# Optimization experiments

Measured on AMD Instinct MI355X. Metric: run time of the kernel, lower is better.

Reference implementation:

```python
import jax, jax.numpy as jnp
import numpy as np

N, FIN, H, M = 20000, 64, 128, 16
EIA, EIR, EIT = 256000, 256000, 100000
EIN = 2 * H + 1          # EGNN edge-mlp input: feats_i | feats_j | rel_dist
EHID = 2 * EIN
NIN = H + M
NHID = 2 * H


def _gat(x_src, x_dst, ei, w_src, w_dst, a_s, a_d, b):
    # PyG GATConv, heads=1: alpha_ij = softmax_i(leaky_relu(a_s.Wx_j + a_d.Wx_i))
    n_dst = x_dst.shape[0]
    h_s = x_src @ w_src                      # [Ns, H]
    h_d = x_dst @ w_dst                      # [Nd, H]
    es = h_s @ a_s                           # [Ns]
    ed = h_d @ a_d                           # [Nd]
    j, i = ei[0], ei[1]                      # src, dst
    e = jax.nn.leaky_relu(es[j] + ed[i], 0.2)
    mx = jax.ops.segment_max(e, i, num_segments=n_dst)
    mx = jnp.where(jnp.isfinite(mx), mx, 0.0)  # guard empty segments
    ex = jnp.exp(e - mx[i])
    den = jax.ops.segment_sum(ex, i, num_segments=n_dst)
    alpha = ex / (den[i] + 1e-16)
    return jax.ops.segment_sum(alpha[:, None] * h_s[j], i, num_segments=n_dst) + b


def _egnn(x, ei, p):
    # EGNN_Sparse: x = [coors(3) | feats], 'add' aggregation, residual feat update
    ew1, eb1, ew2, eb2, cw1, cb1, cw2, cb2, nw1, nb1, nw2, nb2 = p
    coors, feats = x[:, :3], x[:, 3:]
    n = x.shape[0]
    j, i = ei[0], ei[1]
    rel = coors[j] - coors[i]                          # [E, 3] (src - dst)
    rd = jnp.sum(rel * rel, axis=-1, keepdims=True)    # [E, 1]
    m_in = jnp.concatenate([feats[i], feats[j], rd], axis=-1)
    m = jax.nn.silu(jax.nn.silu(m_in @ ew1 + eb1) @ ew2 + eb2)   # [E, M]
    cw = jax.nn.silu(m @ cw1 + cb1) @ cw2 + cb2                  # [E, 1]
    coors_out = coors + jax.ops.segment_sum(cw * rel, i, num_segments=n)
    m_i = jax.ops.segment_sum(m, i, num_segments=n)
    feats_out = feats + jax.nn.silu(jnp.concatenate([feats, m_i], axis=-1) @ nw1 + nb1) @ nw2 + nb2
    return jnp.concatenate([coors_out, feats_out], axis=-1)


def setup_inputs():
    ks = iter(jax.random.split(jax.random.key(0), 48))

    def nrm(shape, s=0.1):
        return jax.random.normal(next(ks), shape, dtype=jnp.float32) * s

    def ridx(shape):
        return jax.random.randint(next(ks), shape, 0, N, dtype=jnp.int32)

    return {
        "x1": nrm((N, FIN), 1.0), "x2": nrm((N, FIN), 1.0),
        "pos1": nrm((N, 3), 1.0), "pos2": nrm((N, 3), 1.0),
        "ei_intra1": ridx((2, EIA)), "ei_intra2": ridx((2, EIA)),
        "ei_12": ridx((2, EIR)), "ei_21": ridx((2, EIR)),
        "ei_int": ridx((2, EIT)),
        "g0_w": nrm((2, FIN, H)), "g0_as": nrm((2, H)), "g0_ad": nrm((2, H)), "g0_b": nrm((2, H)),
        "g1_w": nrm((2, H, H)), "g1_as": nrm((2, H)), "g1_ad": nrm((2, H)), "g1_b": nrm((2, H)),
        "it_ws": nrm((2, 2, H, H)), "it_wd": nrm((2, 2, H, H)),
        "it_as": nrm((2, 2, H)), "it_ad": nrm((2, 2, H)), "it_b": nrm((2, 2, H)),
        "eg_e_w1": nrm((2, 2, EIN, EHID)), "eg_e_b1": nrm((2, 2, EHID)),
        "eg_e_w2": nrm((2, 2, EHID, M)), "eg_e_b2": nrm((2, 2, M)),
        "eg_c_w1": nrm((2, 2, M, 4 * M)), "eg_c_b1": nrm((2, 2, 4 * M)),
        "eg_c_w2": nrm((2, 2, 4 * M, 1)), "eg_c_b2": nrm((2, 2, 1)),
        "eg_n_w1": nrm((2, 2, NIN, NHID)), "eg_n_b1": nrm((2, 2, NHID)),
        "eg_n_w2": nrm((2, 2, NHID, H)), "eg_n_b2": nrm((2, 2, H)),
        "lin_w": nrm((H, 1)), "lin_b": nrm((1,)),
        "aux_w1": nrm((2 * H, H)), "aux_b1": nrm((H,)),
        "aux_w2": nrm((H, 1)), "aux_b2": nrm((1,)),
    }


def reference(x1, x2, pos1, pos2,
              g0_w, g0_as, g0_ad, g0_b, g1_w, g1_as, g1_ad, g1_b,
              it_ws, it_wd, it_as, it_ad, it_b,
              eg_e_w1, eg_e_b1, eg_e_w2, eg_e_b2, eg_c_w1, eg_c_b1, eg_c_w2, eg_c_b2,
              eg_n_w1, eg_n_b1, eg_n_w2, eg_n_b2,
              lin_w, lin_b, aux_w1, aux_b1, aux_w2, aux_b2,
              ei_intra1, ei_intra2, ei_12, ei_21, ei_int):
    n1, n2 = x1.shape[0], x2.shape[0]
    sl1 = jnp.tile(jnp.arange(n1, dtype=ei_intra1.dtype)[None, :], (2, 1))
    sl2 = jnp.tile(jnp.arange(n2, dtype=ei_intra2.dtype)[None, :], (2, 1))
    ei1 = jnp.concatenate([ei_intra1, sl1], axis=1)  # GATConv add_self_loops=True
    ei2 = jnp.concatenate([ei_intra2, sl2], axis=1)
    # intra GAT layers (shared lin for src/dst)
    x1 = jax.nn.relu(_gat(x1, x1, ei1, g0_w[0], g0_w[0], g0_as[0], g0_ad[0], g0_b[0]))
    x2 = jax.nn.relu(_gat(x2, x2, ei2, g0_w[1], g0_w[1], g0_as[1], g0_ad[1], g0_b[1]))
    x1 = jax.nn.relu(_gat(x1, x1, ei1, g1_w[0], g1_w[0], g1_as[0], g1_ad[0], g1_b[0]))
    x2 = jax.nn.relu(_gat(x2, x2, ei2, g1_w[1], g1_w[1], g1_as[1], g1_ad[1], g1_b[1]))
    # inter GAT layers (bipartite, add_self_loops=False)
    for l in range(2):
        nx2 = jax.nn.relu(_gat(x1, x2, ei_12, it_ws[l, 0], it_wd[l, 0], it_as[l, 0], it_ad[l, 0], it_b[l, 0]))
        nx1 = jax.nn.relu(_gat(x2, x1, ei_21, it_ws[l, 1], it_wd[l, 1], it_as[l, 1], it_ad[l, 1], it_b[l, 1]))
        x1, x2 = nx1, nx2
    # EGNN layers (HeteroEGNN hstacks pos only when feat dim == node_dim, i.e. layer 0)
    egp = (eg_e_w1, eg_e_b1, eg_e_w2, eg_e_b2, eg_c_w1, eg_c_b1, eg_c_w2, eg_c_b2,
           eg_n_w1, eg_n_b1, eg_n_w2, eg_n_b2)
    h1 = jnp.concatenate([pos1, x1], axis=-1)
    h2 = jnp.concatenate([pos2, x2], axis=-1)
    for l in range(2):
        h1 = _egnn(h1, ei_intra1, tuple(p[l, 0] for p in egp))
        h2 = _egnn(h2, ei_intra2, tuple(p[l, 1] for p in egp))
    x1, x2 = h1[:, 3:], h2[:, 3:]
    # auxiliary distance head on interacting pairs
    xi = jnp.concatenate([x1[ei_int[0]], x2[ei_int[1]]], axis=-1)
    dist = jax.nn.relu(jax.nn.relu(xi @ aux_w1 + aux_b1) @ aux_w2 + aux_b2)
    return (x1 @ lin_w + lin_b, x2 @ lin_w + lin_b, dist)
```

## Files before the change

### kernel.cpp

```cpp
#include <hip/hip_runtime.h>
#include <hip/hip_bf16.h>
#include <cstdint>
#include <cstddef>

#define NN     20000
#define FIN_D  64
#define H_D    128
#define M_D    16
#define EIA_D  256000
#define EIR_D  256000
#define EIT_D  100000
#define EIN_D  257
#define EHID_D 514
#define NIN_D  144
#define NHID_D 256
#define APAD   544
#define BUPAD  272

typedef short bfrag __attribute__((ext_vector_type(8)));
typedef float ffrag __attribute__((ext_vector_type(4)));

__device__ __forceinline__ float siluf(float x) {
    return x * __builtin_amdgcn_rcpf(1.f + __expf(-x));
}
__device__ __forceinline__ float reluf(float x) { return x > 0.f ? x : 0.f; }
__device__ __forceinline__ unsigned short f2bf(float f) {
    unsigned u = __float_as_uint(f);
    return (unsigned short)((u + 0x7FFFu + ((u >> 16) & 1u)) >> 16);
}
__device__ __forceinline__ float bf2f(unsigned short h) { return __uint_as_float(((unsigned)h) << 16); }
__device__ __forceinline__ float bf_lo(unsigned u) { return __uint_as_float(u << 16); }
__device__ __forceinline__ float bf_hi(unsigned u) { return __uint_as_float(u & 0xFFFF0000u); }
__device__ __forceinline__ unsigned pkbf(float f0, float f1) {
    __hip_bfloat162 h = __float22bfloat162_rn(make_float2(f0, f1));
    return *(unsigned*)&h;
}

__global__ void k_filli(int* p, int v, int n) {
    int i = blockIdx.x * 256 + threadIdx.x; if (i < n) p[i] = v;
}
__global__ void k_iota(int* p, int n) {
    int i = blockIdx.x * 256 + threadIdx.x; if (i < n) p[i] = i;
}
__global__ void k_hist(const int* __restrict__ si, int nE, int* __restrict__ cnt) {
    int e = blockIdx.x * 256 + threadIdx.x; if (e < nE) atomicAdd(&cnt[si[e]], 1);
}
__global__ void k_scan4(const int* __restrict__ cnt4, int n, int* __restrict__ rp4) {
    const int* cnt = cnt4 + (size_t)blockIdx.x * n;
    int* rp = rp4 + (size_t)blockIdx.x * (n + 1);
    __shared__ int tmp[256];
    __shared__ int carry;
    if (threadIdx.x == 0) { carry = 0; rp[0] = 0; }
    __syncthreads();
    for (int base = 0; base < n; base += 256) {
        int i = base + threadIdx.x;
        int v = (i < n) ? cnt[i] : 0;
        tmp[threadIdx.x] = v;
        __syncthreads();
        for (int off = 1; off < 256; off <<= 1) {
            int t = (threadIdx.x >= off) ? tmp[threadIdx.x - off] : 0;
            __syncthreads();
            tmp[threadIdx.x] += t;
            __syncthreads();
        }
        if (i < n) rp[i + 1] = carry + tmp[threadIdx.x];
        __syncthreads();
        if (threadIdx.x == 0) carry += tmp[255];
        __syncthreads();
    }
}
__global__ void k_scatter(const int* __restrict__ sj, const int* __restrict__ si, int nE,
                          const int* __restrict__ rp, int* __restrict__ cursor,
                          int* __restrict__ colj, int* __restrict__ dsti) {
    int e = blockIdx.x * 256 + threadIdx.x;
    if (e >= nE) return;
    int i = si[e];
    int p = rp[i] + atomicAdd(&cursor[i], 1);
    colj[p] = sj[e];
    if (dsti) dsti[p] = i;
}

struct PrepDesc { const float* src; unsigned dstOff; int K, N, Kpad, Npad; };
struct PrepArgs { PrepDesc d[29]; };
__global__ void k_prep(PrepArgs pa, unsigned short* __restrict__ Wt) {
    PrepDesc de = pa.d[blockIdx.x];
    int tot = de.Npad * de.Kpad;
    unsigned short* hi = Wt + de.dstOff;
    unsigned short* lo = hi + tot;
    for (int i = blockIdx.y * 256 + threadIdx.x; i < tot; i += gridDim.y * 256) {
        int n = i / de.Kpad, k = i - n * de.Kpad;
        float v = (n < de.N && k < de.K) ? de.src[(size_t)k * de.N + n] : 0.f;
        unsigned short h = f2bf(v);
        hi[i] = h;
        lo[i] = f2bf(v - bf2f(h));
    }
}

__global__ void k_prep_ew2(const float* __restrict__ eg_e_w2, const float* __restrict__ eg_c_w1,
                           unsigned short* __restrict__ Wf) {
    int pidx = blockIdx.x;
    const float* src = eg_e_w2 + (size_t)pidx * EHID_D * M_D;
    unsigned short* hi = Wf + (size_t)pidx * 8704;
    unsigned short* lo = Wf + 4 * 8704 + (size_t)pidx * 8704;
    for (int idx = threadIdx.x; idx < 8704; idx += 256) {
        int t = idx >> 9, rem = idx & 511;
        int lane = rem >> 3, j2 = rem & 7;
        int k = t * 32 + ((lane >> 4) << 3) + j2;
        int n = lane & 15;
        float v = (k < EHID_D) ? src[(size_t)k * 16 + n] : 0.f;
        unsigned short h = f2bf(v);
        hi[idx] = h;
        lo[idx] = f2bf(v - bf2f(h));
    }
    const float* cw1 = eg_c_w1 + (size_t)pidx * 16 * 64;
    unsigned short* ghi = Wf + 69632 + (size_t)pidx * 4096;
    unsigned short* glo = ghi + 2048;
    for (int idx = threadIdx.x; idx < 2048; idx += 256) {
        int nt = idx >> 9, rem = idx & 511;
        int lane = rem >> 3, j = rem & 7;
        int q = lane >> 4, mm = lane & 15;
        int k = q * 8 + j;
        float v = (k < 16) ? cw1[(size_t)k * 64 + nt * 16 + mm] : 0.f;
        unsigned short h = f2bf(v);
        ghi[idx] = h;
        glo[idx] = f2bf(v - bf2f(h));
    }
}

struct MMJob {
    const float* A; const float* A2;
    const int* gi0; const int* gi1;
    const unsigned short* Wh; const unsigned short* Wl;
    const float* bias; const float* res;
    float* C; unsigned short* C2;
    const float* da; const float* db;
    float* dota; float* dotb;
};
struct MMJobs { MMJob j[4]; };

template<int ACT, bool OBF, int DOT, bool NOC, int KT>
__global__ __launch_bounds__(256) void k_mmf(MMJobs js, int M, int Nc, int ldc, int nbn) {
    constexpr int K = KT * 32;
    __shared__ __align__(16) unsigned short sAh[128 * K];
    const MMJob jb = js.j[blockIdx.z];
    const int tid = threadIdx.x;
    const int bm = blockIdx.x * 128;
    const int wv = tid >> 6, lane = tid & 63;
    const int q = lane >> 4, mm = lane & 15;
    const int sr = tid >> 1;
    const int sks = (tid & 1) * 16;
    const int gm_s = bm + sr;
    const int sgmt = sr >> 4, smm = sr & 15, qb = (tid & 1) * 2;
#pragma unroll
    for (int t = 0; t < KT; ++t) {
        float v[16];
        if (gm_s < M) {
            const float* src = jb.A + (size_t)gm_s * K + t * 32 + sks;
#pragma unroll
            for (int i = 0; i < 4; ++i) {
                float4 t4 = ((const float4*)src)[i];
                v[4 * i] = t4.x; v[4 * i + 1] = t4.y; v[4 * i + 2] = t4.z; v[4 * i + 3] = t4.w;
            }
        } else {
#pragma unroll
            for (int i = 0; i < 16; ++i) v[i] = 0.f;
        }
#pragma unroll
        for (int o = 0; o < 2; ++o) {
            unsigned hw[4];
#pragma unroll
            for (int p = 0; p < 4; ++p)
                hw[p] = pkbf(v[o * 8 + 2 * p], v[o * 8 + 2 * p + 1]);
            int off16 = ((sgmt * KT + t) * 4 + qb + o) * 16 + smm;
            ((uint4*)sAh)[off16] = make_uint4(hw[0], hw[1], hw[2], hw[3]);
        }
    }
    __syncthreads();
    float dra[2][4] = {}, drb[2][4] = {};
    for (int b = 0; b < nbn; ++b) {
        const int bn = b * 64;
        ffrag acc[2][4];
#pragma unroll
        for (int mt = 0; mt < 2; ++mt)
#pragma unroll
            for (int nt = 0; nt < 4; ++nt)
#pragma unroll
                for (int r = 0; r < 4; ++r) acc[mt][nt][r] = 0.f;
#pragma unroll
        for (int t = 0; t < KT; ++t) {
            bfrag bh[4], bl[4];
#pragma unroll
            for (int nt = 0; nt < 4; ++nt) {
                size_t woff = (size_t)(bn + nt * 16 + mm) * K + t * 32 + q * 8;
                bh[nt] = *(const bfrag*)(jb.Wh + woff);
                bl[nt] = *(const bfrag*)(jb.Wl + woff);
            }
#pragma unroll
            for (int mt = 0; mt < 2; ++mt) {
                int off16 = (((wv * 2 + mt) * KT + t) * 4 + q) * 16 + mm;
                bfrag ah = ((const bfrag*)sAh)[off16];
#pragma unroll
                for (int nt = 0; nt < 4; ++nt) {
                    acc[mt][nt] = __builtin_amdgcn_mfma_f32_16x16x32_bf16(ah, bh[nt], acc[mt][nt], 0, 0, 0);
                    acc[mt][nt] = __builtin_amdgcn_mfma_f32_16x16x32_bf16(ah, bl[nt], acc[mt][nt], 0, 0, 0);
                }
            }
        }
        if (DOT >= 1) {
            float dav[4], dbv[4];
#pragma unroll
            for (int nt = 0; nt < 4; ++nt) {
                int gn = bn + nt * 16 + mm;
                dav[nt] = (gn < Nc) ? jb.da[gn] : 0.f;
                if (DOT == 2) dbv[nt] = (gn < Nc) ? jb.db[gn] : 0.f;
            }
#pragma unroll
            for (int mt = 0; mt < 2; ++mt)
#pragma unroll
                for (int r = 0; r < 4; ++r)
#pragma unroll
                    for (int nt = 0; nt < 4; ++nt) {
                        dra[mt][r] += acc[mt][nt][r] * dav[nt];
                        if (DOT == 2) drb[mt][r] += acc[mt][nt][r] * dbv[nt];
                    }
        }
        const bool doC2 = jb.C2 != nullptr;
        if (!NOC || doC2) {
#pragma unroll
            for (int mt = 0; mt < 2; ++mt) {
#pragma unroll
                for (int nt = 0; nt < 4; ++nt) {
                    int gn = bn + nt * 16 + mm;
                    bool inb = gn < Nc;
                    bool padz = OBF && !NOC && !inb && gn < ldc;
                    if (!inb && !padz) continue;
#pragma unroll
                    for (int r = 0; r < 4; ++r) {
                        int gm = bm + wv * 32 + mt * 16 + q * 4 + r;
                        if (gm >= M) continue;
                        if (padz) {
                            ((unsigned short*)jb.C)[(size_t)gm * ldc + gn] = 0;
                            continue;
                        }
                        float vv = acc[mt][nt][r];
                        if (jb.bias) vv += jb.bias[gn];
                        if (ACT == 1) vv = reluf(vv);
                        if (ACT == 2) vv = siluf(vv);
                        if (!NOC) {
                            if (OBF) ((unsigned short*)jb.C)[(size_t)gm * ldc + gn] = f2bf(vv);
                            else jb.C[(size_t)gm * ldc + gn] = vv;
                        }
                        if (doC2) jb.C2[(size_t)gm * ldc + gn] = f2bf(vv);
                    }
                }
            }
        }
    }
    if (DOT >= 1) {
#pragma unroll
        for (int mt = 0; mt < 2; ++mt)
#pragma unroll
            for (int r = 0; r < 4; ++r) {
                float sa = dra[mt][r];
                sa += __shfl_xor(sa, 1); sa += __shfl_xor(sa, 2);
                sa += __shfl_xor(sa, 4); sa += __shfl_xor(sa, 8);
                float sb = 0.f;
                if (DOT == 2) {
                    sb = drb[mt][r];
                    sb += __shfl_xor(sb, 1); sb += __shfl_xor(sb, 2);
                    sb += __shfl_xor(sb, 4); sb += __shfl_xor(sb, 8);
                }
                int gm = bm + wv * 32 + mt * 16 + q * 4 + r;
                if (mm == 0 && gm < M) {
                    jb.dota[gm] = sa;
                    if (DOT == 2) jb.dotb[gm] = sb;
                }
            }
    }
}

template<int ACT, bool RES, bool GATHER>
__global__ __launch_bounds__(256) void k_mm(MMJobs js, int M, int Nc, int K, int Kpad, int ldc, int s2) {
    __shared__ __align__(16) unsigned short sAh[128 * 32];
    __shared__ __align__(16) unsigned short sAl[128 * 32];
    const MMJob jb = js.j[blockIdx.z];
    const int tid = threadIdx.x;
    const int bm = blockIdx.x * 128, bn = blockIdx.y * 64;
    const int wv = tid >> 6, lane = tid & 63;
    ffrag acc[2][4];
#pragma unroll
    for (int mt = 0; mt < 2; ++mt)
#pragma unroll
        for (int nt = 0; nt < 4; ++nt)
#pragma unroll
            for (int r = 0; r < 4; ++r) acc[mt][nt][r] = 0.f;
    const int sr = tid >> 1;
    const int sks = (tid & 1) * 16;
    const int gm_s = bm + sr;
    const int sgmt = sr >> 4, smm = sr & 15, qb = (tid & 1) * 2;
    int gidx0 = 0, gidx1 = 0;
    if (GATHER && gm_s < M) { gidx0 = jb.gi0[gm_s]; gidx1 = jb.gi1[gm_s]; }
    const int q = lane >> 4, mm = lane & 15;

    for (int k0 = 0; k0 < Kpad; k0 += 32) {
        float v[16];
        bool valid = (gm_s < M) && (k0 + sks < K);
        if (valid) {
            const float* src;
            int kk = k0 + sks;
            if (GATHER) src = (kk < 128) ? (jb.A + (size_t)gidx0 * 128 + kk)
                                         : (jb.A2 + (size_t)gidx1 * s2 + (kk - 128));
            else src = jb.A + (size_t)gm_s * K + kk;
#pragma unroll
            for (int i = 0; i < 4; ++i) {
                float4 t4 = ((const float4*)src)[i];
                v[4 * i] = t4.x; v[4 * i + 1] = t4.y; v[4 * i + 2] = t4.z; v[4 * i + 3] = t4.w;
            }
        } else {
#pragma unroll
            for (int i = 0; i < 16; ++i) v[i] = 0.f;
        }
#pragma unroll
        for (int o = 0; o < 2; ++o) {
            unsigned hw[4], lw[4];
#pragma unroll
            for (int p = 0; p < 4; ++p) {
                float f0 = v[o * 8 + 2 * p], f1 = v[o * 8 + 2 * p + 1];
                unsigned short h0 = f2bf(f0), h1 = f2bf(f1);
                unsigned short l0 = f2bf(f0 - bf2f(h0)), l1 = f2bf(f1 - bf2f(h1));
                hw[p] = (unsigned)h0 | ((unsigned)h1 << 16);
                lw[p] = (unsigned)l0 | ((unsigned)l1 << 16);
            }
            int off16 = (sgmt * 4 + qb + o) * 16 + smm;
            ((uint4*)sAh)[off16] = make_uint4(hw[0], hw[1], hw[2], hw[3]);
            ((uint4*)sAl)[off16] = make_uint4(lw[0], lw[1], lw[2], lw[3]);
        }
        __syncthreads();
        bfrag bh[4], bl[4];
#pragma unroll
        for (int nt = 0; nt < 4; ++nt) {
            size_t woff = (size_t)(bn + nt * 16 + mm) * Kpad + k0 + q * 8;
            bh[nt] = *(const bfrag*)(jb.Wh + woff);
            bl[nt] = *(const bfrag*)(jb.Wl + woff);
        }
#pragma unroll
        for (int mt = 0; mt < 2; ++mt) {
            int off16 = ((wv * 2 + mt) * 4 + q) * 16 + mm;
            bfrag ah = ((const bfrag*)sAh)[off16];
            bfrag al = ((const bfrag*)sAl)[off16];
#pragma unroll
            for (int nt = 0; nt < 4; ++nt) {
                acc[mt][nt] = __builtin_amdgcn_mfma_f32_16x16x32_bf16(ah, bh[nt], acc[mt][nt], 0, 0, 0);
                acc[mt][nt] = __builtin_amdgcn_mfma_f32_16x16x32_bf16(ah, bl[nt], acc[mt][nt], 0, 0, 0);
                acc[mt][nt] = __builtin_amdgcn_mfma_f32_16x16x32_bf16(al, bh[nt], acc[mt][nt], 0, 0, 0);
            }
        }
        __syncthreads();
    }
#pragma unroll
    for (int mt = 0; mt < 2; ++mt) {
#pragma unroll
        for (int nt = 0; nt < 4; ++nt) {
            int gn = bn + nt * 16 + mm;
            if (gn >= Nc) continue;
#pragma unroll
            for (int r = 0; r < 4; ++r) {
                int gm = bm + wv * 32 + mt * 16 + q * 4 + r;
                if (gm >= M) continue;
                float vv = acc[mt][nt][r];
                if (jb.bias) vv += jb.bias[gn];
                if (ACT == 1) vv = reluf(vv);
                if (ACT == 2) vv = siluf(vv);
                if (RES) vv += jb.res[(size_t)gm * Nc + gn];
                jb.C[(size_t)gm * ldc + gn] = vv;
            }
        }
    }
}

__global__ void k_nodescore(const float* __restrict__ x, const float* __restrict__ wv,
                            const float* __restrict__ b, float* __restrict__ o, int n) {
    int w = blockIdx.x * 4 + (threadIdx.x >> 6);
    int lane = threadIdx.x & 63;
    if (w >= n) return;
    const float* r = x + (size_t)w * H_D;
    float s = r[lane] * wv[lane] + r[lane + 64] * wv[lane + 64];
#pragma unroll
    for (int off = 32; off; off >>= 1) s += __shfl_xor(s, off);
    if (lane == 0) o[w] = s + b[0];
}

struct GatJob {
    const int* rp; const int* cj; int hasSelf;
    const float* es; const float* ed;
    const unsigned* h16; const float* bias; float* out;
};
__global__ __launch_bounds__(256) void k_gat2(GatJob j0, GatJob j1, int N) {
    const GatJob jb = blockIdx.y ? j1 : j0;
    int node = blockIdx.x * 4 + (threadIdx.x >> 6);
    int lane = threadIdx.x & 63;
    if (node >= N) return;
    int start = jb.rp[node], end = jb.rp[node + 1];
    float edi = jb.ed[node];
    float den = 0.f, a0 = 0.f, a1 = 0.f;
    int p = start;
    for (; p + 4 <= end; p += 4) {
        int j[4]; float e[4]; unsigned u[4];
#pragma unroll
        for (int x = 0; x < 4; ++x) j[x] = jb.cj[p + x];
#pragma unroll
        for (int x = 0; x < 4; ++x) { e[x] = jb.es[j[x]]; u[x] = jb.h16[(size_t)j[x] * 64 + lane]; }
#pragma unroll
        for (int x = 0; x < 4; ++x) {
            float v = e[x] + edi;
            v = v < 0.f ? 0.2f * v : v;
            float ex = __expf(v);
            den += ex;
            a0 += ex * bf_lo(u[x]);
            a1 += ex * bf_hi(u[x]);
        }
    }
    for (; p < end; ++p) {
        int j = jb.cj[p];
        float v = jb.es[j] + edi;
        v = v < 0.f ? 0.2f * v : v;
        float ex = __expf(v);
        den += ex;
        unsigned u = jb.h16[(size_t)j * 64 + lane];
        a0 += ex * bf_lo(u);
        a1 += ex * bf_hi(u);
    }
    if (jb.hasSelf) {
        float v = jb.es[node] + edi;
        v = v < 0.f ? 0.2f * v : v;
        float ex = __expf(v);
        den += ex;
        unsigned u = jb.h16[(size_t)node * 64 + lane];
        a0 += ex * bf_lo(u);
        a1 += ex * bf_hi(u);
    }
    float inv = 1.f / (den + 1e-16f);
    float2 o;
    o.x = reluf(a0 * inv + jb.bias[2 * lane]);
    o.y = reluf(a1 * inv + jb.bias[2 * lane + 1]);
    ((float2*)(jb.out + (size_t)node * H_D))[lane] = o;
}

struct EJob {
    const int* dsti; const int* cj;
    const unsigned* A16; const unsigned* Bp; const float* coors;
    const float* w_rd;
    const unsigned short* Wfh; const unsigned short* Wfl;
    const unsigned short* Wgh; const unsigned short* Wgl;
    const float* eb2; const float* cb1;
    const float* cw2; const float* cb2;
    unsigned short* me16; float* cvec;
};
__global__ __launch_bounds__(256) void k_edge2(EJob e0, EJob e1, int nE) {
    const EJob jb = blockIdx.y ? e1 : e0;
    __shared__ __align__(16) float s_w[APAD];
    __shared__ float s_cb1[64], s_cw2[64], s_eb2[16];
    __shared__ __align__(16) float sM[4][16][20];
    for (int i = threadIdx.x; i < APAD; i += 256)
        s_w[i] = (i < EHID_D) ? jb.w_rd[i] : 0.f;
    if (threadIdx.x < 64) { s_cb1[threadIdx.x] = jb.cb1[threadIdx.x]; s_cw2[threadIdx.x] = jb.cw2[threadIdx.x]; }
    if (threadIdx.x < 16) s_eb2[threadIdx.x] = jb.eb2[threadIdx.x];
    __syncthreads();
    const float cb2v = jb.cb2[0];
    const int wv = threadIdx.x >> 6, lane = threadIdx.x & 63;
    const int q = lane >> 4, mm = lane & 15;
    const int ebase = blockIdx.x * 64 + wv * 16;
    const int e = ebase + mm;
    const bool ev = e < nE;
    int ii = ev ? jb.dsti[e] : 0;
    int jj = ev ? jb.cj[e] : 0;
    float dx = jb.coors[(size_t)jj * 3]     - jb.coors[(size_t)ii * 3];
    float dy = jb.coors[(size_t)jj * 3 + 1] - jb.coors[(size_t)ii * 3 + 1];
    float dz = jb.coors[(size_t)jj * 3 + 2] - jb.coors[(size_t)ii * 3 + 2];
    float rd = dx * dx + dy * dy + dz * dz;
    const unsigned* Ar = jb.A16 + (size_t)ii * BUPAD;
    const unsigned* Br = jb.Bp + (size_t)jj * BUPAD;
    ffrag acc = {0.f, 0.f, 0.f, 0.f};
#pragma unroll 4
    for (int t = 0; t < 17; ++t) {
        int ks = t * 32 + q * 8;
        int ku = ks >> 1;
        uint4 au = *(const uint4*)(Ar + ku);
        uint4 bu = *(const uint4*)(Br + ku);
        float4 w0 = *(const float4*)(s_w + ks);
        float4 w1 = *(const float4*)(s_w + ks + 4);
        float g[8];
        g[0] = siluf(bf_lo(au.x) + bf_lo(bu.x) + rd * w0.x);
        g[1] = siluf(bf_hi(au.x) + bf_hi(bu.x) + rd * w0.y);
        g[2] = siluf(bf_lo(au.y) + bf_lo(bu.y) + rd * w0.z);
        g[3] = siluf(bf_hi(au.y) + bf_hi(bu.y) + rd * w0.w);
        g[4] = siluf(bf_lo(au.z) + bf_lo(bu.z) + rd * w1.x);
        g[5] = siluf(bf_hi(au.z) + bf_hi(bu.z) + rd * w1.y);
        g[6] = siluf(bf_lo(au.w) + bf_lo(bu.w) + rd * w1.z);
        g[7] = siluf(bf_hi(au.w) + bf_hi(bu.w) + rd * w1.w);
        bfrag ah;
        unsigned* ahp = (unsigned*)&ah;
        ahp[0] = pkbf(g[0], g[1]);
        ahp[1] = pkbf(g[2], g[3]);
        ahp[2] = pkbf(g[4], g[5]);
        ahp[3] = pkbf(g[6], g[7]);
        bfrag bh = *(const bfrag*)(jb.Wfh + (size_t)(t * 64 + lane) * 8);
        bfrag bl = *(const bfrag*)(jb.Wfl + (size_t)(t * 64 + lane) * 8);
        acc = __builtin_amdgcn_mfma_f32_16x16x32_bf16(ah, bh, acc, 0, 0, 0);
        acc = __builtin_amdgcn_mfma_f32_16x16x32_bf16(ah, bl, acc, 0, 0, 0);
    }
#pragma unroll
    for (int r = 0; r < 4; ++r) {
        int erow = q * 4 + r;
        float me = siluf(acc[r] + s_eb2[mm]);
        sM[wv][erow][mm] = me;
        int e2 = ebase + erow;
        if (e2 < nE) jb.me16[(size_t)e2 * 16 + mm] = f2bf(me);
    }
    bfrag ag;
    unsigned* agp = (unsigned*)&ag;
    if (q < 2) {
        float4 m0 = *(const float4*)&sM[wv][mm][q * 8];
        float4 m1 = *(const float4*)&sM[wv][mm][q * 8 + 4];
        agp[0] = pkbf(m0.x, m0.y);
        agp[1] = pkbf(m0.z, m0.w);
        agp[2] = pkbf(m1.x, m1.y);
        agp[3] = pkbf(m1.z, m1.w);
    } else {
        agp[0] = agp[1] = agp[2] = agp[3] = 0u;
    }
    float part[4] = {0.f, 0.f, 0.f, 0.f};
#pragma unroll
    for (int nt = 0; nt < 4; ++nt) {
        bfrag gh = *(const bfrag*)(jb.Wgh + (size_t)(nt * 64 + lane) * 8);
        bfrag gl = *(const bfrag*)(jb.Wgl + (size_t)(nt * 64 + lane) * 8);
        ffrag a2 = {0.f, 0.f, 0.f, 0.f};
        a2 = __builtin_amdgcn_mfma_f32_16x16x32_bf16(ag, gh, a2, 0, 0, 0);
        a2 = __builtin_amdgcn_mfma_f32_16x16x32_bf16(ag, gl, a2, 0, 0, 0);
        int n = nt * 16 + mm;
        float c1 = s_cb1[n], c2 = s_cw2[n];
#pragma unroll
        for (int r = 0; r < 4; ++r) part[r] += siluf(a2[r] + c1) * c2;
    }
#pragma unroll
    for (int r = 0; r < 4; ++r) {
        part[r] += __shfl_xor(part[r], 1);
        part[r] += __shfl_xor(part[r], 2);
        part[r] += __shfl_xor(part[r], 4);
        part[r] += __shfl_xor(part[r], 8);
    }
    int srcl = (lane >> 2) << 4;
    float cand0 = __shfl(part[0], srcl);
    float cand1 = __shfl(part[1], srcl);
    float cand2 = __shfl(part[2], srcl);
    float cand3 = __shfl(part[3], srcl);
    if (lane < 16) {
        int rr = lane & 3;
        float cwv = (rr == 0 ? cand0 : rr == 1 ? cand1 : rr == 2 ? cand2 : cand3) + cb2v;
        int e3 = ebase + lane;
        if (e3 < nE) {
            jb.cvec[(size_t)e3 * 3]     = cwv * dx;
            jb.cvec[(size_t)e3 * 3 + 1] = cwv * dy;
            jb.cvec[(size_t)e3 * 3 + 2] = cwv * dz;
        }
    }
}

struct SJob {
    const int* rp; const unsigned short* me16; const float* cvec;
    const float* coors; float* coorsOut; float* macc;
};
__global__ __launch_bounds__(256) void k_seg2(SJob s0, SJob s1, int N) {
    const SJob jb = blockIdx.y ? s1 : s0;
    int node = blockIdx.x * 4 + (threadIdx.x >> 6);
    int lane = threadIdx.x & 63;
    if (node >= N) return;
    int s = jb.rp[node], en = jb.rp[node + 1];
    int x = lane >> 4, c = lane & 15;
    float msum = 0.f, csum = 0.f;
    for (int p = s + x; p < en; p += 4) {
        msum += bf2f(jb.me16[(size_t)p * 16 + c]);
        if (c < 3) csum += jb.cvec[(size_t)p * 3 + c];
    }
    msum += __shfl_xor(msum, 16); msum += __shfl_xor(msum, 32);
    csum += __shfl_xor(csum, 16); csum += __shfl_xor(csum, 32);
    if (lane < 16) jb.macc[(size_t)node * M_D + lane] = msum;
    if (lane < 3) jb.coorsOut[(size_t)node * 3 + lane] = jb.coors[(size_t)node * 3 + lane] + csum;
}

__global__ void k_dist(const float* __restrict__ Hb, const float* __restrict__ w2,
                       const float* __restrict__ b2, float* __restrict__ dist, int nE) {
    int e = blockIdx.x * 4 + (threadIdx.x >> 6);
    int lane = threadIdx.x & 63;
    if (e >= nE) return;
    const float* r = Hb + (size_t)e * H_D;
    float s = r[lane] * w2[lane] + r[lane + 64] * w2[lane + 64];
#pragma unroll
    for (int off = 32; off; off >>= 1) s += __shfl_xor(s, off);
    if (lane == 0) dist[e] = reluf(s + b2[0]);
}

extern "C" void kernel_launch(void* const* d_in, const int* in_sizes, int n_in,
                              void* d_out, int out_size, void* d_ws, size_t ws_size,
                              hipStream_t stream) {
    const float* x1_in = (const float*)d_in[0];
    const float* x2_in = (const float*)d_in[1];
    const float* pos1  = (const float*)d_in[2];
    const float* pos2  = (const float*)d_in[3];
    const int* ei_intra1 = (const int*)d_in[4];
    const int* ei_intra2 = (const int*)d_in[5];
    const int* ei_12 = (const int*)d_in[6];
    const int* ei_21 = (const int*)d_in[7];
    const int* ei_int = (const int*)d_in[8];
    const float* g0_w  = (const float*)d_in[9];
    const float* g0_as = (const float*)d_in[10];
    const float* g0_ad = (const float*)d_in[11];
    const float* g0_b  = (const float*)d_in[12];
    const float* g1_w  = (const float*)d_in[13];
    const float* g1_as = (const float*)d_in[14];
    const float* g1_ad = (const float*)d_in[15];
    const float* g1_b  = (const float*)d_in[16];
    const float* it_ws = (const float*)d_in[17];
    const float* it_wd = (const float*)d_in[18];
    const float* it_as = (const float*)d_in[19];
    const float* it_ad = (const float*)d_in[20];
    const float* it_b  = (const float*)d_in[21];
    const float* eg_e_w1 = (const float*)d_in[22];
    const float* eg_e_b1 = (const float*)d_in[23];
    const float* eg_e_w2 = (const float*)d_in[24];
    const float* eg_e_b2 = (const float*)d_in[25];
    const float* eg_c_w1 = (const float*)d_in[26];
    const float* eg_c_b1 = (const float*)d_in[27];
    const float* eg_c_w2 = (const float*)d_in[28];
    const float* eg_c_b2 = (const float*)d_in[29];
    const float* eg_n_w1 = (const float*)d_in[30];
    const float* eg_n_b1 = (const float*)d_in[31];
    const float* eg_n_w2 = (const float*)d_in[32];
    const float* eg_n_b2 = (const float*)d_in[33];
    const float* lin_w = (const float*)d_in[34];
    const float* lin_b = (const float*)d_in[35];
    const float* aux_w1 = (const float*)d_in[36];
    const float* aux_b1 = (const float*)d_in[37];
    const float* aux_w2 = (const float*)d_in[38];
    const float* aux_b2 = (const float*)d_in[39];
    float* dout = (float*)d_out;

    float* wsf = (float*)d_ws;
    size_t off = 0;
    auto alloc = [&](size_t nfl) { float* p = wsf + off; off += (nfl + 255) & ~(size_t)255; return p; };
    float* x1a = alloc((size_t)NN * H_D);
    float* x2a = alloc((size_t)NN * H_D);
    float* x1b = alloc((size_t)NN * H_D);
    float* x2b = alloc((size_t)NN * H_D);
    float* esed = alloc(4 * NN);
    float* es1 = esed, *es2 = esed + NN, *ed1 = esed + 2 * NN, *ed2 = esed + 3 * NN;
    float* co1a = alloc(NN * 3);
    float* co1b = alloc(NN * 3);
    float* co2a = alloc(NN * 3);
    float* co2b = alloc(NN * 3);
    float* macc1 = alloc((size_t)NN * M_D);
    float* macc2 = alloc((size_t)NN * M_D);
    unsigned* A16a = (unsigned*)alloc((size_t)NN * BUPAD);
    unsigned* B16a = (unsigned*)alloc((size_t)NN * BUPAD);
    unsigned* A16b = (unsigned*)alloc((size_t)NN * BUPAD);
    unsigned* B16b = (unsigned*)alloc((size_t)NN * BUPAD);
    unsigned* h16a = (unsigned*)alloc((size_t)NN * 64);
    unsigned* h16b = (unsigned*)alloc((size_t)NN * 64);
    int* cnt4 = (int*)alloc(4 * NN);
    int* rp4 = (int*)alloc(4 * (NN + 1));
    int* cjI1 = (int*)alloc(EIA_D);
    int* cjI2 = (int*)alloc(EIA_D);
    int* cj12 = (int*)alloc(EIR_D);
    int* cj21 = (int*)alloc(EIR_D);
    int* dstI1 = (int*)alloc(EIA_D);
    int* dstI2 = (int*)alloc(EIA_D);
    int* iota = (int*)alloc(NN);
    unsigned short* Wt = (unsigned short*)alloc(1100000);
    unsigned short* Wf = (unsigned short*)alloc(45000);
    unsigned short* me16a = (unsigned short*)alloc((size_t)EIA_D * 8);
    unsigned short* me16b = (unsigned short*)alloc((size_t)EIA_D * 8);
    float* cveca = alloc((size_t)EIA_D * 3);
    float* cvecb = alloc((size_t)EIA_D * 3);
    float* nh1 = (float*)B16a;
    float* nh2 = (float*)B16b;
    float* Hb  = (float*)A16a;

    const int N = NN, H = H_D;
    int gNW = (N + 3) / 4;
    int gEA = (EIA_D + 255) / 256;

    PrepArgs pa;
    unsigned woffs[29], wsz[29];
    unsigned wo = 0;
    int wi = 0;
    auto addw = [&](const float* src, int K, int Ncols) {
        int Kpad = (K + 31) & ~31;
        int Npad = (Ncols + 63) & ~63;
        pa.d[wi] = {src, wo, K, Ncols, Kpad, Npad};
        woffs[wi] = wo; wsz[wi] = (unsigned)(Npad * Kpad);
        wo += 2u * Npad * Kpad;
        ++wi;
    };
    addw(g0_w, FIN_D, H);
    addw(g0_w + FIN_D * H, FIN_D, H);
    addw(g1_w, H, H);
    addw(g1_w + H * H, H, H);
    for (int p = 0; p < 4; ++p) addw(it_ws + (size_t)p * H * H, H, H);
    for (int p = 0; p < 4; ++p) addw(it_wd + (size_t)p * H * H, H, H);
    for (int p = 0; p < 4; ++p) {
        const float* ew1 = eg_e_w1 + (size_t)p * EIN_D * EHID_D;
        addw(ew1, H, EHID_D);
        addw(ew1 + (size_t)H * EHID_D, H, EHID_D);
    }
    for (int p = 0; p < 4; ++p) addw(eg_n_w1 + (size_t)p * NIN_D * NHID_D, NIN_D, NHID_D);
    for (int p = 0; p < 4; ++p) addw(eg_n_w2 + (size_t)p * NHID_D * H, NHID_D, H);
    addw(aux_w1, 2 * H, H);
    k_prep<<<dim3(29, 16), 256, 0, stream>>>(pa, Wt);
    k_prep_ew2<<<4, 256, 0, stream>>>(eg_e_w2, eg_c_w1, Wf);
    auto WH = [&](int i) { return (const unsigned short*)(Wt + woffs[i]); };
    auto WL = [&](int i) { return (const unsigned short*)(Wt + woffs[i] + wsz[i]); };

    k_filli<<<(4 * N + 255) / 256, 256, 0, stream>>>(cnt4, 0, 4 * N);
    k_iota<<<(N + 255) / 256, 256, 0, stream>>>(iota, N);
    k_hist<<<gEA, 256, 0, stream>>>(ei_intra1 + EIA_D, EIA_D, cnt4);
    k_hist<<<gEA, 256, 0, stream>>>(ei_intra2 + EIA_D, EIA_D, cnt4 + N);
    k_hist<<<gEA, 256, 0, stream>>>(ei_12 + EIR_D, EIR_D, cnt4 + 2 * N);
    k_hist<<<gEA, 256, 0, stream>>>(ei_21 + EIR_D, EIR_D, cnt4 + 3 * N);
    k_scan4<<<4, 256, 0, stream>>>(cnt4, N, rp4);
    k_filli<<<(4 * N + 255) / 256, 256, 0, stream>>>(cnt4, 0, 4 * N);
    const int* rpI1 = rp4;
    const int* rpI2 = rp4 + (N + 1);
    const int* rp12 = rp4 + 2 * (N + 1);
    const int* rp21 = rp4 + 3 * (N + 1);
    k_scatter<<<gEA, 256, 0, stream>>>(ei_intra1, ei_intra1 + EIA_D, EIA_D, rpI1, cnt4, cjI1, dstI1);
    k_scatter<<<gEA, 256, 0, stream>>>(ei_intra2, ei_intra2 + EIA_D, EIA_D, rpI2, cnt4 + N, cjI2, dstI2);
    k_scatter<<<gEA, 256, 0, stream>>>(ei_12, ei_12 + EIR_D, EIR_D, rp12, cnt4 + 2 * N, cj12, nullptr);
    k_scatter<<<gEA, 256, 0, stream>>>(ei_21, ei_21 + EIR_D, EIR_D, rp21, cnt4 + 3 * N, cj21, nullptr);

    const int MB = (N + 127) / 128;
    MMJobs js{};

    auto intraL = [&](auto kt_tag, const float* xa, const float* xb, int wa, int wb,
                      const float* as_a, const float* ad_a, const float* as_b, const float* ad_b,
                      const float* b_a, const float* b_b, float* oa, float* ob) {
        constexpr int KT = decltype(kt_tag)::value;
        js.j[0] = {xa, nullptr, nullptr, nullptr, WH(wa), WL(wa), nullptr, nullptr,
                   nullptr, (unsigned short*)h16a, as_a, ad_a, es1, ed1};
        js.j[1] = {xb, nullptr, nullptr, nullptr, WH(wb), WL(wb), nullptr, nullptr,
                   nullptr, (unsigned short*)h16b, as_b, ad_b, es2, ed2};
        k_mmf<0, false, 2, true, KT><<<dim3(MB, 1, 2), 256, 0, stream>>>(js, N, H, H, 2);
        GatJob g0{rpI1, cjI1, 1, es1, ed1, h16a, b_a, oa};
        GatJob g1{rpI2, cjI2, 1, es2, ed2, h16b, b_b, ob};
        k_gat2<<<dim3(gNW, 2), 256, 0, stream>>>(g0, g1, N);
    };

    intraL(std::integral_constant<int, 2>{}, x1_in, x2_in, 0, 1,
           g0_as, g0_ad, g0_as + H, g0_ad + H, g0_b, g0_b + H, x1a, x2a);
    const float* cx1 = x1a;
    const float* cx2 = x2a;
    intraL(std::integral_constant<int, 4>{}, cx1, cx2, 2, 3,
           g1_as, g1_ad, g1_as + H, g1_ad + H, g1_b, g1_b + H, x1b, x2b);
    cx1 = x1b; cx2 = x2b;

    {
        float* outs1[2] = {x1a, x1b};
        float* outs2[2] = {x2a, x2b};
        for (int l = 0; l < 2; ++l) {
            int p0 = l * 2 + 0, p1 = l * 2 + 1;
            float* o2 = outs2[l];
            float* o1 = outs1[l];
            js.j[0] = {cx1, nullptr, nullptr, nullptr, WH(4 + p0), WL(4 + p0), nullptr, nullptr,
                       nullptr, (unsigned short*)h16a, it_as + p0 * H, nullptr, es1, nullptr};
            js.j[1] = {cx2, nullptr, nullptr, nullptr, WH(4 + p1), WL(4 + p1), nullptr, nullptr,
                       nullptr, (unsigned short*)h16b, it_as + p1 * H, nullptr, es2, nullptr};
            js.j[2] = {cx2, nullptr, nullptr, nullptr, WH(8 + p0), WL(8 + p0), nullptr, nullptr,
                       nullptr, nullptr, it_ad + p0 * H, nullptr, ed1, nullptr};
            js.j[3] = {cx1, nullptr, nullptr, nullptr, WH(8 + p1), WL(8 + p1), nullptr, nullptr,
                       nullptr, nullptr, it_ad + p1 * H, nullptr, ed2, nullptr};
            k_mmf<0, false, 1, true, 4><<<dim3(MB, 1, 4), 256, 0, stream>>>(js, N, H, H, 2);
            GatJob g0{rp12, cj12, 0, es1, ed1, h16a, it_b + p0 * H, o2};
            GatJob g1{rp21, cj21, 0, es2, ed2, h16b, it_b + p1 * H, o1};
            k_gat2<<<dim3(gNW, 2), 256, 0, stream>>>(g0, g1, N);
            cx1 = o1; cx2 = o2;
        }
    }

    auto egnn_pair = [&](const float* f1, const float* f2, const float* c1, const float* c2,
                         int l, float* fo1, float* fo2, float* co1, float* co2) {
        int p0 = 2 * l, p1 = 2 * l + 1;
        js.j[0] = {f1, nullptr, nullptr, nullptr, WH(12 + 2 * p0), WL(12 + 2 * p0),
                   eg_e_b1 + p0 * EHID_D, nullptr, (float*)A16a, nullptr, nullptr, nullptr, nullptr, nullptr};
        js.j[1] = {f1, nullptr, nullptr, nullptr, WH(13 + 2 * p0), WL(13 + 2 * p0),
                   nullptr, nullptr, (float*)B16a, nullptr, nullptr, nullptr, nullptr, nullptr};
        js.j[2] = {f2, nullptr, nullptr, nullptr, WH(12 + 2 * p1), WL(12 + 2 * p1),
                   eg_e_b1 + p1 * EHID_D, nullptr, (float*)A16b, nullptr, nullptr, nullptr, nullptr, nullptr};
        js.j[3] = {f2, nullptr, nullptr, nullptr, WH(13 + 2 * p1), WL(13 + 2 * p1),
                   nullptr, nullptr, (float*)B16b, nullptr, nullptr, nullptr, nullptr, nullptr};
        k_mmf<0, true, 0, false, 4><<<dim3(MB, 1, 4), 256, 0, stream>>>(js, N, EHID_D, APAD, 9);
        const float* ew1a = eg_e_w1 + (size_t)p0 * EIN_D * EHID_D;
        const float* ew1b = eg_e_w1 + (size_t)p1 * EIN_D * EHID_D;
        EJob e0{dstI1, cjI1, A16a, B16a, c1, ew1a + (size_t)256 * EHID_D,
                Wf + (size_t)p0 * 8704, Wf + 4 * 8704 + (size_t)p0 * 8704,
                Wf + 69632 + (size_t)p0 * 4096, Wf + 69632 + (size_t)p0 * 4096 + 2048,
                eg_e_b2 + p0 * M_D, eg_c_b1 + p0 * 64,
                eg_c_w2 + p0 * 64, eg_c_b2 + p0, me16a, cveca};
        EJob e1{dstI2, cjI2, A16b, B16b, c2, ew1b + (size_t)256 * EHID_D,
                Wf + (size_t)p1 * 8704, Wf + 4 * 8704 + (size_t)p1 * 8704,
                Wf + 69632 + (size_t)p1 * 4096, Wf + 69632 + (size_t)p1 * 4096 + 2048,
                eg_e_b2 + p1 * M_D, eg_c_b1 + p1 * 64,
                eg_c_w2 + p1 * 64, eg_c_b2 + p1, me16b, cvecb};
        k_edge2<<<dim3((EIA_D + 63) / 64, 2), 256, 0, stream>>>(e0, e1, EIA_D);
        SJob s0{rpI1, me16a, cveca, c1, co1, macc1};
        SJob s1{rpI2, me16b, cvecb, c2, co2, macc2};
        k_seg2<<<dim3(gNW, 2), 256, 0, stream>>>(s0, s1, N);
        js.j[0] = {f1, macc1, iota, iota, WH(20 + p0), WL(20 + p0),
                   eg_n_b1 + p0 * NHID_D, nullptr, nh1, nullptr, nullptr, nullptr, nullptr, nullptr};
        js.j[1] = {f2, macc2, iota, iota, WH(20 + p1), WL(20 + p1),
                   eg_n_b1 + p1 * NHID_D, nullptr, nh2, nullptr, nullptr, nullptr, nullptr, nullptr};
        k_mm<2, false, true><<<dim3(MB, 4, 2), 256, 0, stream>>>(js, N, NHID_D, NIN_D, 160, NHID_D, M_D);
        js.j[0] = {nh1, nullptr, nullptr, nullptr, WH(24 + p0), WL(24 + p0),
                   eg_n_b2 + p0 * H, f1, fo1, nullptr, nullptr, nullptr, nullptr, nullptr};
        js.j[1] = {nh2, nullptr, nullptr, nullptr, WH(24 + p1), WL(24 + p1),
                   eg_n_b2 + p1 * H, f2, fo2, nullptr, nullptr, nullptr, nullptr, nullptr};
        k_mm<0, true, false><<<dim3(MB, 2, 2), 256, 0, stream>>>(js, N, H, NHID_D, NHID_D, H, 0);
    };
    egnn_pair(cx1, cx2, pos1, pos2, 0, x1a, x2a, co1a, co2a);
    cx1 = x1a; cx2 = x2a;
    egnn_pair(cx1, cx2, co1a, co2a, 1, x1b, x2b, co1b, co2b);
    cx1 = x1b; cx2 = x2b;

    k_nodescore<<<gNW, 256, 0, stream>>>(cx1, lin_w, lin_b, dout, N);
    k_nodescore<<<gNW, 256, 0, stream>>>(cx2, lin_w, lin_b, dout + N, N);
    js.j[0] = {cx1, cx2, ei_int, ei_int + EIT_D, WH(28), WL(28),
               aux_b1, nullptr, Hb, nullptr, nullptr, nullptr, nullptr, nullptr};
    k_mm<1, false, true><<<dim3((EIT_D + 127) / 128, 2, 1), 256, 0, stream>>>(
        js, EIT_D, H, 2 * H, 2 * H, H, H_D);
    k_dist<<<(EIT_D + 3) / 4, 256, 0, stream>>>(Hb, aux_w2, aux_b2, dout + 2 * N, EIT_D);
}
```

Baseline: 1.434 ms.

## Route remaining matmuls through full-K LDS-staged k_mmf kernel with gather/residual support

Extends k_mmf with gather and residual template options and a runtime active-K bound, then replaces the older k_mm kernel (which split A into hi/lo bf16 and ran three MFMAs per step) for the EGNN node MLP and the aux distance matmul. The A tile is staged once for the whole K and each block loops over all N columns instead of launching separate column blocks, so gathered rows are not re-read per column block. It also drops the A low-part correction, which lowers precision on those matmuls, and uses larger shared memory per block, which may reduce occupancy.

```diff
diff --git a/kernel.cpp b/kernel.cpp
--- a/kernel.cpp
+++ b/kernel.cpp
@@ -2,6 +2,7 @@
 #include <hip/hip_bf16.h>
 #include <cstdint>
 #include <cstddef>
+#include <type_traits>
 
 #define NN     20000
 #define FIN_D  64
@@ -138,8 +139,9 @@
 };
 struct MMJobs { MMJob j[4]; };
 
-template<int ACT, bool OBF, int DOT, bool NOC, int KT>
-__global__ __launch_bounds__(256) void k_mmf(MMJobs js, int M, int Nc, int ldc, int nbn) {
+template<int ACT, bool OBF, int DOT, bool NOC, int KT, bool GATHER, bool RES>
+__global__ __launch_bounds__(256) void k_mmf(MMJobs js, int M, int Nc, int ldc, int nbn,
+                                             int Kact, int s2) {
     constexpr int K = KT * 32;
     __shared__ __align__(16) unsigned short sAh[128 * K];
     const MMJob jb = js.j[blockIdx.z];
@@ -151,11 +153,18 @@
     const int sks = (tid & 1) * 16;
     const int gm_s = bm + sr;
     const int sgmt = sr >> 4, smm = sr & 15, qb = (tid & 1) * 2;
+    int gidx0 = 0, gidx1 = 0;
+    if (GATHER && gm_s < M) { gidx0 = jb.gi0[gm_s]; gidx1 = jb.gi1[gm_s]; }
 #pragma unroll
     for (int t = 0; t < KT; ++t) {
         float v[16];
-        if (gm_s < M) {
-            const float* src = jb.A + (size_t)gm_s * K + t * 32 + sks;
+        int kk = t * 32 + sks;
+        bool valid = (gm_s < M) && (kk < Kact);
+        if (valid) {
+            const float* src;
+            if (GATHER) src = (kk < 128) ? (jb.A + (size_t)gidx0 * 128 + kk)
+                                         : (jb.A2 + (size_t)gidx1 * s2 + (kk - 128));
+            else src = jb.A + (size_t)gm_s * K + kk;
 #pragma unroll
             for (int i = 0; i < 4; ++i) {
                 float4 t4 = ((const float4*)src)[i];
@@ -246,6 +255,7 @@
                         if (jb.bias) vv += jb.bias[gn];
                         if (ACT == 1) vv = reluf(vv);
                         if (ACT == 2) vv = siluf(vv);
+                        if (RES) vv += jb.res[(size_t)gm * Nc + gn];
                         if (!NOC) {
                             if (OBF) ((unsigned short*)jb.C)[(size_t)gm * ldc + gn] = f2bf(vv);
                             else jb.C[(size_t)gm * ldc + gn] = vv;
@@ -276,105 +286,6 @@
                     if (DOT == 2) jb.dotb[gm] = sb;
                 }
             }
-    }
-}
-
-template<int ACT, bool RES, bool GATHER>
-__global__ __launch_bounds__(256) void k_mm(MMJobs js, int M, int Nc, int K, int Kpad, int ldc, int s2) {
-    __shared__ __align__(16) unsigned short sAh[128 * 32];
-    __shared__ __align__(16) unsigned short sAl[128 * 32];
-    const MMJob jb = js.j[blockIdx.z];
-    const int tid = threadIdx.x;
-    const int bm = blockIdx.x * 128, bn = blockIdx.y * 64;
-    const int wv = tid >> 6, lane = tid & 63;
-    ffrag acc[2][4];
-#pragma unroll
-    for (int mt = 0; mt < 2; ++mt)
-#pragma unroll
-        for (int nt = 0; nt < 4; ++nt)
-#pragma unroll
-            for (int r = 0; r < 4; ++r) acc[mt][nt][r] = 0.f;
-    const int sr = tid >> 1;
-    const int sks = (tid & 1) * 16;
-    const int gm_s = bm + sr;
-    const int sgmt = sr >> 4, smm = sr & 15, qb = (tid & 1) * 2;
-    int gidx0 = 0, gidx1 = 0;
-    if (GATHER && gm_s < M) { gidx0 = jb.gi0[gm_s]; gidx1 = jb.gi1[gm_s]; }
-    const int q = lane >> 4, mm = lane & 15;
-
-    for (int k0 = 0; k0 < Kpad; k0 += 32) {
-        float v[16];
-        bool valid = (gm_s < M) && (k0 + sks < K);
-        if (valid) {
-            const float* src;
-            int kk = k0 + sks;
-            if (GATHER) src = (kk < 128) ? (jb.A + (size_t)gidx0 * 128 + kk)
-                                         : (jb.A2 + (size_t)gidx1 * s2 + (kk - 128));
-            else src = jb.A + (size_t)gm_s * K + kk;
-#pragma unroll
-            for (int i = 0; i < 4; ++i) {
-                float4 t4 = ((const float4*)src)[i];
-                v[4 * i] = t4.x; v[4 * i + 1] = t4.y; v[4 * i + 2] = t4.z; v[4 * i + 3] = t4.w;
-            }
-        } else {
-#pragma unroll
-            for (int i = 0; i < 16; ++i) v[i] = 0.f;
-        }
-#pragma unroll
-        for (int o = 0; o < 2; ++o) {
-            unsigned hw[4], lw[4];
-#pragma unroll
-            for (int p = 0; p < 4; ++p) {
-                float f0 = v[o * 8 + 2 * p], f1 = v[o * 8 + 2 * p + 1];
-                unsigned short h0 = f2bf(f0), h1 = f2bf(f1);
-                unsigned short l0 = f2bf(f0 - bf2f(h0)), l1 = f2bf(f1 - bf2f(h1));
-                hw[p] = (unsigned)h0 | ((unsigned)h1 << 16);
-                lw[p] = (unsigned)l0 | ((unsigned)l1 << 16);
-            }
-            int off16 = (sgmt * 4 + qb + o) * 16 + smm;
-            ((uint4*)sAh)[off16] = make_uint4(hw[0], hw[1], hw[2], hw[3]);
-            ((uint4*)sAl)[off16] = make_uint4(lw[0], lw[1], lw[2], lw[3]);
-        }
-        __syncthreads();
-        bfrag bh[4], bl[4];
-#pragma unroll
-        for (int nt = 0; nt < 4; ++nt) {
-            size_t woff = (size_t)(bn + nt * 16 + mm) * Kpad + k0 + q * 8;
-            bh[nt] = *(const bfrag*)(jb.Wh + woff);
-            bl[nt] = *(const bfrag*)(jb.Wl + woff);
-        }
-#pragma unroll
-        for (int mt = 0; mt < 2; ++mt) {
-            int off16 = ((wv * 2 + mt) * 4 + q) * 16 + mm;
-            bfrag ah = ((const bfrag*)sAh)[off16];
-            bfrag al = ((const bfrag*)sAl)[off16];
-#pragma unroll
-            for (int nt = 0; nt < 4; ++nt) {
-                acc[mt][nt] = __builtin_amdgcn_mfma_f32_16x16x32_bf16(ah, bh[nt], acc[mt][nt], 0, 0, 0);
-                acc[mt][nt] = __builtin_amdgcn_mfma_f32_16x16x32_bf16(ah, bl[nt], acc[mt][nt], 0, 0, 0);
-                acc[mt][nt] = __builtin_amdgcn_mfma_f32_16x16x32_bf16(al, bh[nt], acc[mt][nt], 0, 0, 0);
-            }
-        }
-        __syncthreads();
-    }
-#pragma unroll
-    for (int mt = 0; mt < 2; ++mt) {
-#pragma unroll
-        for (int nt = 0; nt < 4; ++nt) {
-            int gn = bn + nt * 16 + mm;
-            if (gn >= Nc) continue;
-#pragma unroll
-            for (int r = 0; r < 4; ++r) {
-                int gm = bm + wv * 32 + mt * 16 + q * 4 + r;
-                if (gm >= M) continue;
-                float vv = acc[mt][nt][r];
-                if (jb.bias) vv += jb.bias[gn];
-                if (ACT == 1) vv = reluf(vv);
-                if (ACT == 2) vv = siluf(vv);
-                if (RES) vv += jb.res[(size_t)gm * Nc + gn];
-                jb.C[(size_t)gm * ldc + gn] = vv;
-            }
-        }
     }
 }
 
@@ -748,7 +659,8 @@
                    nullptr, (unsigned short*)h16a, as_a, ad_a, es1, ed1};
         js.j[1] = {xb, nullptr, nullptr, nullptr, WH(wb), WL(wb), nullptr, nullptr,
                    nullptr, (unsigned short*)h16b, as_b, ad_b, es2, ed2};
-        k_mmf<0, false, 2, true, KT><<<dim3(MB, 1, 2), 256, 0, stream>>>(js, N, H, H, 2);
+        k_mmf<0, false, 2, true, KT, false, false><<<dim3(MB, 1, 2), 256, 0, stream>>>(
+            js, N, H, H, 2, KT * 32, 0);
         GatJob g0{rpI1, cjI1, 1, es1, ed1, h16a, b_a, oa};
         GatJob g1{rpI2, cjI2, 1, es2, ed2, h16b, b_b, ob};
         k_gat2<<<dim3(gNW, 2), 256, 0, stream>>>(g0, g1, N);
@@ -777,7 +689,8 @@
                        nullptr, nullptr, it_ad + p0 * H, nullptr, ed1, nullptr};
             js.j[3] = {cx1, nullptr, nullptr, nullptr, WH(8 + p1), WL(8 + p1), nullptr, nullptr,
                        nullptr, nullptr, it_ad + p1 * H, nullptr, ed2, nullptr};
-            k_mmf<0, false, 1, true, 4><<<dim3(MB, 1, 4), 256, 0, stream>>>(js, N, H, H, 2);
+            k_mmf<0, false, 1, true, 4, false, false><<<dim3(MB, 1, 4), 256, 0, stream>>>(
+                js, N, H, H, 2, 128, 0);
             GatJob g0{rp12, cj12, 0, es1, ed1, h16a, it_b + p0 * H, o2};
             GatJob g1{rp21, cj21, 0, es2, ed2, h16b, it_b + p1 * H, o1};
             k_gat2<<<dim3(gNW, 2), 256, 0, stream>>>(g0, g1, N);
@@ -796,7 +709,8 @@
                    eg_e_b1 + p1 * EHID_D, nullptr, (float*)A16b, nullptr, nullptr, nullptr, nullptr, nullptr};
         js.j[3] = {f2, nullptr, nullptr, nullptr, WH(13 + 2 * p1), WL(13 + 2 * p1),
                    nullptr, nullptr, (float*)B16b, nullptr, nullptr, nullptr, nullptr, nullptr};
-        k_mmf<0, true, 0, false, 4><<<dim3(MB, 1, 4), 256, 0, stream>>>(js, N, EHID_D, APAD, 9);
+        k_mmf<0, true, 0, false, 4, false, false><<<dim3(MB, 1, 4), 256, 0, stream>>>(
+            js, N, EHID_D, APAD, 9, 128, 0);
         const float* ew1a = eg_e_w1 + (size_t)p0 * EIN_D * EHID_D;
         const float* ew1b = eg_e_w1 + (size_t)p1 * EIN_D * EHID_D;
         EJob e0{dstI1, cjI1, A16a, B16a, c1, ew1a + (size_t)256 * EHID_D,
@@ -817,23 +731,25 @@
                    eg_n_b1 + p0 * NHID_D, nullptr, nh1, nullptr, nullptr, nullptr, nullptr, nullptr};
         js.j[1] = {f2, macc2, iota, iota, WH(20 + p1), WL(20 + p1),
                    eg_n_b1 + p1 * NHID_D, nullptr, nh2, nullptr, nullptr, nullptr, nullptr, nullptr};
-        k_mm<2, false, true><<<dim3(MB, 4, 2), 256, 0, stream>>>(js, N, NHID_D, NIN_D, 160, NHID_D, M_D);
+        k_mmf<2, false, 0, false, 5, true, false><<<dim3(MB, 1, 2), 256, 0, stream>>>(
+            js, N, NHID_D, NHID_D, 4, NIN_D, M_D);
         js.j[0] = {nh1, nullptr, nullptr, nullptr, WH(24 + p0), WL(24 + p0),
                    eg_n_b2 + p0 * H, f1, fo1, nullptr, nullptr, nullptr, nullptr, nullptr};
         js.j[1] = {nh2, nullptr, nullptr, nullptr, WH(24 + p1), WL(24 + p1),
                    eg_n_b2 + p1 * H, f2, fo2, nullptr, nullptr, nullptr, nullptr, nullptr};
-        k_mm<0, true, false><<<dim3(MB, 2, 2), 256, 0, stream>>>(js, N, H, NHID_D, NHID_D, H, 0);
+        k_mmf<0, false, 0, false, 8, false, true><<<dim3(MB, 1, 2), 256, 0, stream>>>(
+            js, N, H, H, 2, NHID_D, 0);
     };
     egnn_pair(cx1, cx2, pos1, pos2, 0, x1a, x2a, co1a, co2a);
     cx1 = x1a; cx2 = x2a;
     egnn_pair(cx1, cx2, co1a, co2a, 1, x1b, x2b, co1b, co2b);
     cx1 = x1b; cx2 = x2b;
 
-    k_nodescore<<<gNW, 256, 0, stream>>>(cx1, lin_w, lin_b, dout, N);
-    k_nodescore<<<gNW, 256, 0, stream>>>(cx2, lin_w, lin_b, dout + N, N);
+    k_nodescore<<<gNW, 2 * 128, 0, stream>>>(cx1, lin_w, lin_b, dout, N);
+    k_nodescore<<<gNW, 2 * 128, 0, stream>>>(cx2, lin_w, lin_b, dout + N, N);
     js.j[0] = {cx1, cx2, ei_int, ei_int + EIT_D, WH(28), WL(28),
                aux_b1, nullptr, Hb, nullptr, nullptr, nullptr, nullptr, nullptr};
-    k_mm<1, false, true><<<dim3((EIT_D + 127) / 128, 2, 1), 256, 0, stream>>>(
-        js, EIT_D, H, 2 * H, 2 * H, H, H_D);
+    k_mmf<1, false, 0, false, 8, true, false><<<dim3((EIT_D + 127) / 128, 1, 1), 256, 0, stream>>>(
+        js, EIT_D, H, H, 2, 2 * H, H_D);
     k_dist<<<(EIT_D + 3) / 4, 256, 0, stream>>>(Hb, aux_w2, aux_b2, dout + 2 * N, EIT_D);
 }
```

New measurement: 1.500 ms. 1.05x slower.
